# Performance work log

Measured on AMD Instinct MI355X. Metric: run time of the kernel, lower is better.

The kernel has to match this reference:

```python
import jax, jax.numpy as jnp
import numpy as np

EXPERT_NUM = 64
EXPERT_USE = 8
AUX_LOSS_LAMBDA = 0.01


def setup_inputs() -> dict:
    key = jax.random.key(0)
    k1, k2 = jax.random.split(key)
    h = jax.random.normal(k1, (4, 4096, 2048), dtype=jnp.float32)
    # nn.Linear(embed_dim, expert_num) weight: [expert_num, embed_dim], ~U(-1/sqrt(d), 1/sqrt(d))
    bound = 1.0 / np.sqrt(2048.0)
    W = jax.random.uniform(k2, (EXPERT_NUM, 2048), dtype=jnp.float32,
                           minval=-bound, maxval=bound)
    return {"h": h, "W": W}


def reference(h, W):
    b, s, d = h.shape
    hf = h.reshape(-1, d)                              # [b*s, d]
    logits = jnp.einsum('nd,ed->ne', hf, W)            # [b*s, E]
    scores = jax.nn.softmax(logits, axis=-1)           # [b*s, E]
    expert_scores, expert_ids = jax.lax.top_k(scores, EXPERT_USE)  # [b*s, k]
    expert_weight = expert_scores / jnp.sum(expert_scores, axis=-1, keepdims=True)
    # L2 load-balance aux loss (training mode, lambda > 0)
    seq_probs = scores.reshape(b, s, EXPERT_NUM).mean(axis=1)      # [b, E]
    aux_loss = jnp.mean(jnp.sum(seq_probs ** 2, axis=-1)) * EXPERT_NUM * AUX_LOSS_LAMBDA
    return expert_ids, expert_weight, aux_loss
```

## Files before the change

### kernel.cpp

```cpp
#include <hip/hip_runtime.h>
#include <math.h>

#define NTOK 16384
#define DIM 2048
#define NEXP 64
#define TOPK 8
#define BT 32
#define KC 64
#define NCHUNK (DIM / KC)
#define PADK 68
#define NBLK (NTOK / BT)

typedef float f2 __attribute__((ext_vector_type(2)));
typedef float f4 __attribute__((ext_vector_type(4)));

__device__ __forceinline__ f2 pk_mul(f2 a, f2 b) {
    f2 d; asm("v_pk_mul_f32 %0, %1, %2" : "=v"(d) : "v"(a), "v"(b)); return d;
}
__device__ __forceinline__ f2 pk_add(f2 a, f2 b) {
    f2 d; asm("v_pk_add_f32 %0, %1, %2" : "=v"(d) : "v"(a), "v"(b)); return d;
}

__global__ __launch_bounds__(256, 2) void moe_gate_np(
    const float* __restrict__ h, const float* __restrict__ W,
    float* __restrict__ out, float* __restrict__ wsum)
{
#pragma clang fp contract(off)
    __shared__ float sA[BT * PADK];
    __shared__ float sB[NEXP * PADK];
    __shared__ float lg[BT][NEXP + 2];

    const int tid = threadIdx.x;
    const int blk = blockIdx.x;
    const long tok0 = (long)blk * BT;
    const float* hA = h + tok0 * DIM;

    const int rA = tid >> 3;
    const int cA = (tid & 7) * 8;
    const int rB = tid >> 2;
    const int cB = (tid & 3) * 16;

    f4 pa[2], pb[4];
    #pragma unroll
    for (int q = 0; q < 2; ++q) pa[q] = *(const f4*)(hA + (long)rA * DIM + cA + 4 * q);
    #pragma unroll
    for (int q = 0; q < 4; ++q) pb[q] = *(const f4*)(W + (long)rB * DIM + cB + 4 * q);

    const int tx = tid & 15;
    const int ty = tid >> 4;

    f2 axy[2][4], azw[2][4];
    #pragma unroll
    for (int i = 0; i < 2; ++i)
        #pragma unroll
        for (int j = 0; j < 4; ++j) { axy[i][j] = (f2)(0.f); azw[i][j] = (f2)(0.f); }

    for (int kc = 0; kc < NCHUNK; ++kc) {
        __syncthreads();
        #pragma unroll
        for (int q = 0; q < 2; ++q) *(f4*)&sA[rA * PADK + cA + 4 * q] = pa[q];
        #pragma unroll
        for (int q = 0; q < 4; ++q) *(f4*)&sB[rB * PADK + cB + 4 * q] = pb[q];
        __syncthreads();

        if (kc + 1 < NCHUNK) {
            const long ko = (long)(kc + 1) * KC;
            #pragma unroll
            for (int q = 0; q < 2; ++q) pa[q] = *(const f4*)(hA + (long)rA * DIM + ko + cA + 4 * q);
            #pragma unroll
            for (int q = 0; q < 4; ++q) pb[q] = *(const f4*)(W + (long)rB * DIM + ko + cB + 4 * q);
        }

        #pragma unroll
        for (int s = 0; s < 4; ++s) {
            f2 alo[2][4], ahi[2][4], blo[4][4], bhi[4][4];
            #pragma unroll
            for (int i = 0; i < 2; ++i) {
                const float* base = &sA[(ty + 16 * i) * PADK + s * 16];
                #pragma unroll
                for (int v = 0; v < 4; ++v) {
                    f4 a = *(const f4*)(base + 4 * v);
                    alo[i][v] = __builtin_shufflevector(a, a, 0, 1);
                    ahi[i][v] = __builtin_shufflevector(a, a, 2, 3);
                }
            }
            #pragma unroll
            for (int j = 0; j < 4; ++j) {
                const float* base = &sB[(tx + 16 * j) * PADK + s * 16];
                #pragma unroll
                for (int v = 0; v < 4; ++v) {
                    f4 b = *(const f4*)(base + 4 * v);
                    blo[j][v] = __builtin_shufflevector(b, b, 0, 1);
                    bhi[j][v] = __builtin_shufflevector(b, b, 2, 3);
                }
            }
            #pragma unroll
            for (int i = 0; i < 2; ++i)
                #pragma unroll
                for (int j = 0; j < 4; ++j) {
                    f2 t;
                    t = pk_add(pk_mul(alo[i][3], blo[j][3]), axy[i][j]);
                    t = pk_add(pk_mul(alo[i][2], blo[j][2]), t);
                    t = pk_add(pk_mul(alo[i][1], blo[j][1]), t);
                    axy[i][j] = pk_add(pk_mul(alo[i][0], blo[j][0]), t);
                    t = pk_add(pk_mul(ahi[i][3], bhi[j][3]), azw[i][j]);
                    t = pk_add(pk_mul(ahi[i][2], bhi[j][2]), t);
                    t = pk_add(pk_mul(ahi[i][1], bhi[j][1]), t);
                    azw[i][j] = pk_add(pk_mul(ahi[i][0], bhi[j][0]), t);
                }
        }
    }

    #pragma unroll
    for (int i = 0; i < 2; ++i)
        #pragma unroll
        for (int j = 0; j < 4; ++j) {
            f2 s2 = pk_add(axy[i][j], azw[i][j]);
            lg[ty + 16 * i][tx + 16 * j] = s2.x + s2.y;
        }
    __syncthreads();

    const int lane = tid & 63;
    const int wv   = tid >> 6;
    float auxacc = 0.f;

    for (int tt = 0; tt < 8; ++tt) {
        const int t = wv * 8 + tt;
        const float s = lg[t][lane];

        float m = s;
        #pragma unroll
        for (int off = 32; off >= 1; off >>= 1)
            m = fmaxf(m, __shfl_xor(m, off));

        const float p = expf(s - m);
        lg[t][lane] = p;
        __asm__ volatile("" ::: "memory");

        float r0 = lg[t][0], r1 = lg[t][1], r2 = lg[t][2], r3 = lg[t][3];
        float r4 = lg[t][4], r5 = lg[t][5], r6 = lg[t][6], r7 = lg[t][7];
        #pragma unroll
        for (int i = 1; i < 8; ++i) {
            r0 += lg[t][8 * i + 0]; r1 += lg[t][8 * i + 1];
            r2 += lg[t][8 * i + 2]; r3 += lg[t][8 * i + 3];
            r4 += lg[t][8 * i + 4]; r5 += lg[t][8 * i + 5];
            r6 += lg[t][8 * i + 6]; r7 += lg[t][8 * i + 7];
        }
        const float S = ((r0 + r1) + (r2 + r3)) + ((r4 + r5) + (r6 + r7));

        const float score = p / S;
        auxacc += score;

        float cv = score;
        float myv = 0.f;
        int   myi = 0;
        #pragma unroll
        for (int i = 0; i < TOPK; ++i) {
            float v = cv;
            int idx = lane;
            #pragma unroll
            for (int off = 32; off >= 1; off >>= 1) {
                float v2 = __shfl_xor(v, off);
                int   i2 = __shfl_xor(idx, off);
                if (v2 > v || (v2 == v && i2 < idx)) { v = v2; idx = i2; }
            }
            if (lane == i)   { myv = v; myi = idx; }
            if (lane == idx) cv = -1.f;
        }

        float S8 = 0.f;
        #pragma unroll
        for (int r = 0; r < TOPK; ++r) S8 += __shfl(myv, r);

        if (lane < TOPK) {
            const long o = (tok0 + t) * TOPK + lane;
            out[o]                     = (float)myi;
            out[(long)NTOK * TOPK + o] = myv / S8;
        }
    }

    const int b = blk >> 7;
    atomicAdd(&wsum[b * NEXP + lane], auxacc);
}

__global__ void aux_finish(const float* __restrict__ wsum, float* __restrict__ out)
{
    const int lane = threadIdx.x;
    float a = 0.f;
    #pragma unroll
    for (int b = 0; b < 4; ++b) {
        const float v = wsum[b * NEXP + lane] * (1.0f / 4096.0f);
        a = fmaf(v, v, a);
    }
    #pragma unroll
    for (int off = 32; off >= 1; off >>= 1)
        a += __shfl_xor(a, off);
    if (lane == 0)
        out[2L * NTOK * TOPK] = a * 0.25f * (float)NEXP * 0.01f;
}

extern "C" void kernel_launch(void* const* d_in, const int* in_sizes, int n_in,
                              void* d_out, int out_size, void* d_ws, size_t ws_size,
                              hipStream_t stream) {
    const float* h = (const float*)d_in[0];
    const float* W = (const float*)d_in[1];
    float* out  = (float*)d_out;
    float* wsum = (float*)d_ws;

    hipMemsetAsync(d_ws, 0, 1024, stream);
    moe_gate_np<<<NBLK, 256, 0, stream>>>(h, W, out, wsum);
    aux_finish<<<1, 64, 0, stream>>>(wsum, out);
}
```

Before: 165.5 us.

## Shrink gate kernel to single-wave blocks of 16 tokens with 32-wide K chunks

Each block becomes one 64-thread wave that handles 16 tokens instead of 32. Each thread now computes a 4x4 output tile, and the K chunk shrinks to 32 with matching padding, so the block-wide barriers involve only a single wave. The same wave then runs the softmax and top-k for all 16 tokens in sequence. In exchange, each block re-reads the whole expert weight matrix for half as many tokens, the grid holds fewer total waves to hide memory latency, and the serial per-token epilogue gets longer.

```diff
diff --git a/kernel.cpp b/kernel.cpp
--- a/kernel.cpp
+++ b/kernel.cpp
@@ -5,10 +5,10 @@
 #define DIM 2048
 #define NEXP 64
 #define TOPK 8
-#define BT 32
-#define KC 64
+#define BT 16
+#define KC 32
 #define NCHUNK (DIM / KC)
-#define PADK 68
+#define PADK 36
 #define NBLK (NTOK / BT)
 
 typedef float f2 __attribute__((ext_vector_type(2)));
@@ -21,7 +21,7 @@
     f2 d; asm("v_pk_add_f32 %0, %1, %2" : "=v"(d) : "v"(a), "v"(b)); return d;
 }
 
-__global__ __launch_bounds__(256, 2) void moe_gate_np(
+__global__ __launch_bounds__(64, 1) void moe_gate_np(
     const float* __restrict__ h, const float* __restrict__ W,
     float* __restrict__ out, float* __restrict__ wsum)
 {
@@ -35,55 +35,47 @@
     const long tok0 = (long)blk * BT;
     const float* hA = h + tok0 * DIM;
 
-    const int rA = tid >> 3;
-    const int cA = (tid & 7) * 8;
-    const int rB = tid >> 2;
-    const int cB = (tid & 3) * 16;
-
-    f4 pa[2], pb[4];
-    #pragma unroll
-    for (int q = 0; q < 2; ++q) pa[q] = *(const f4*)(hA + (long)rA * DIM + cA + 4 * q);
-    #pragma unroll
-    for (int q = 0; q < 4; ++q) pb[q] = *(const f4*)(W + (long)rB * DIM + cB + 4 * q);
+    const int srow = tid >> 3;
+    const int scol = (tid & 7) * 4;
+
+    f4 pa[2], pb[8];
+    #pragma unroll
+    for (int q = 0; q < 2; ++q)
+        pa[q] = *(const f4*)(hA + (long)(8 * q + srow) * DIM + scol);
+    #pragma unroll
+    for (int q = 0; q < 8; ++q)
+        pb[q] = *(const f4*)(W + (long)(8 * q + srow) * DIM + scol);
 
     const int tx = tid & 15;
     const int ty = tid >> 4;
 
-    f2 axy[2][4], azw[2][4];
-    #pragma unroll
-    for (int i = 0; i < 2; ++i)
+    f2 axy[4][4], azw[4][4];
+    #pragma unroll
+    for (int i = 0; i < 4; ++i)
         #pragma unroll
         for (int j = 0; j < 4; ++j) { axy[i][j] = (f2)(0.f); azw[i][j] = (f2)(0.f); }
 
     for (int kc = 0; kc < NCHUNK; ++kc) {
         __syncthreads();
         #pragma unroll
-        for (int q = 0; q < 2; ++q) *(f4*)&sA[rA * PADK + cA + 4 * q] = pa[q];
-        #pragma unroll
-        for (int q = 0; q < 4; ++q) *(f4*)&sB[rB * PADK + cB + 4 * q] = pb[q];
+        for (int q = 0; q < 2; ++q) *(f4*)&sA[(8 * q + srow) * PADK + scol] = pa[q];
+        #pragma unroll
+        for (int q = 0; q < 8; ++q) *(f4*)&sB[(8 * q + srow) * PADK + scol] = pb[q];
         __syncthreads();
 
         if (kc + 1 < NCHUNK) {
             const long ko = (long)(kc + 1) * KC;
             #pragma unroll
-            for (int q = 0; q < 2; ++q) pa[q] = *(const f4*)(hA + (long)rA * DIM + ko + cA + 4 * q);
-            #pragma unroll
-            for (int q = 0; q < 4; ++q) pb[q] = *(const f4*)(W + (long)rB * DIM + ko + cB + 4 * q);
-        }
-
-        #pragma unroll
-        for (int s = 0; s < 4; ++s) {
-            f2 alo[2][4], ahi[2][4], blo[4][4], bhi[4][4];
-            #pragma unroll
-            for (int i = 0; i < 2; ++i) {
-                const float* base = &sA[(ty + 16 * i) * PADK + s * 16];
-                #pragma unroll
-                for (int v = 0; v < 4; ++v) {
-                    f4 a = *(const f4*)(base + 4 * v);
-                    alo[i][v] = __builtin_shufflevector(a, a, 0, 1);
-                    ahi[i][v] = __builtin_shufflevector(a, a, 2, 3);
-                }
-            }
+            for (int q = 0; q < 2; ++q)
+                pa[q] = *(const f4*)(hA + (long)(8 * q + srow) * DIM + ko + scol);
+            #pragma unroll
+            for (int q = 0; q < 8; ++q)
+                pb[q] = *(const f4*)(W + (long)(8 * q + srow) * DIM + ko + scol);
+        }
+
+        #pragma unroll
+        for (int s = 0; s < 2; ++s) {
+            f2 blo[4][4], bhi[4][4];
             #pragma unroll
             for (int j = 0; j < 4; ++j) {
                 const float* base = &sB[(tx + 16 * j) * PADK + s * 16];
@@ -95,37 +87,46 @@
                 }
             }
             #pragma unroll
-            for (int i = 0; i < 2; ++i)
+            for (int i = 0; i < 4; ++i) {
+                f2 alo[4], ahi[4];
+                const float* base = &sA[(ty + 4 * i) * PADK + s * 16];
+                #pragma unroll
+                for (int v = 0; v < 4; ++v) {
+                    f4 a = *(const f4*)(base + 4 * v);
+                    alo[v] = __builtin_shufflevector(a, a, 0, 1);
+                    ahi[v] = __builtin_shufflevector(a, a, 2, 3);
+                }
                 #pragma unroll
                 for (int j = 0; j < 4; ++j) {
                     f2 t;
-                    t = pk_add(pk_mul(alo[i][3], blo[j][3]), axy[i][j]);
-                    t = pk_add(pk_mul(alo[i][2], blo[j][2]), t);
-                    t = pk_add(pk_mul(alo[i][1], blo[j][1]), t);
-                    axy[i][j] = pk_add(pk_mul(alo[i][0], blo[j][0]), t);
-                    t = pk_add(pk_mul(ahi[i][3], bhi[j][3]), azw[i][j]);
-                    t = pk_add(pk_mul(ahi[i][2], bhi[j][2]), t);
-                    t = pk_add(pk_mul(ahi[i][1], bhi[j][1]), t);
-                    azw[i][j] = pk_add(pk_mul(ahi[i][0], bhi[j][0]), t);
+                    t = pk_add(pk_mul(alo[3], blo[j][3]), axy[i][j]);
+                    t = pk_add(pk_mul(alo[2], blo[j][2]), t);
+                    t = pk_add(pk_mul(alo[1], blo[j][1]), t);
+                    axy[i][j] = pk_add(pk_mul(alo[0], blo[j][0]), t);
+                    t = pk_add(pk_mul(ahi[3], bhi[j][3]), azw[i][j]);
+                    t = pk_add(pk_mul(ahi[2], bhi[j][2]), t);
+                    t = pk_add(pk_mul(ahi[1], bhi[j][1]), t);
+                    azw[i][j] = pk_add(pk_mul(ahi[0], bhi[j][0]), t);
                 }
+            }
         }
     }
 
-    #pragma unroll
-    for (int i = 0; i < 2; ++i)
+    __syncthreads();
+    #pragma unroll
+    for (int i = 0; i < 4; ++i)
         #pragma unroll
         for (int j = 0; j < 4; ++j) {
             f2 s2 = pk_add(axy[i][j], azw[i][j]);
-            lg[ty + 16 * i][tx + 16 * j] = s2.x + s2.y;
+            lg[ty + 4 * i][tx + 16 * j] = s2.x + s2.y;
         }
     __syncthreads();
 
-    const int lane = tid & 63;
-    const int wv   = tid >> 6;
+    const int lane = tid;
     float auxacc = 0.f;
 
-    for (int tt = 0; tt < 8; ++tt) {
-        const int t = wv * 8 + tt;
+    for (int tt = 0; tt < BT; ++tt) {
+        const int t = tt;
         const float s = lg[t][lane];
 
         float m = s;
@@ -179,7 +180,7 @@
         }
     }
 
-    const int b = blk >> 7;
+    const int b = blk >> 8;
     atomicAdd(&wsum[b * NEXP + lane], auxacc);
 }
 
@@ -208,6 +209,6 @@
     float* wsum = (float*)d_ws;
 
     hipMemsetAsync(d_ws, 0, 1024, stream);
-    moe_gate_np<<<NBLK, 256, 0, stream>>>(h, W, out, wsum);
+    moe_gate_np<<<NBLK, 64, 0, stream>>>(h, W, out, wsum);
     aux_finish<<<1, 64, 0, stream>>>(wsum, out);
 }
```

Result: slower. 206.8 us (+25.0%).

## Load h operands directly from global into registers, bypassing shared memory

Applied to the files above, without the earlier changes.

Removes the shared-memory staging tile for the token activations. Each thread now loads its own two token rows straight from global memory into registers, with a one-step register prefetch, while W stays staged through LDS. This cuts LDS traffic and footprint for A. In exchange, 16 lanes now read the same row addresses, which gives uncoalesced or broadcast-dependent global loads and higher register pressure.

```diff
diff --git a/kernel.cpp b/kernel.cpp
--- a/kernel.cpp
+++ b/kernel.cpp
@@ -8,6 +8,7 @@
 #define BT 32
 #define KC 64
 #define NCHUNK (DIM / KC)
+#define NST (DIM / 16)
 #define PADK 68
 #define NBLK (NTOK / BT)
 
@@ -19,6 +20,15 @@
 }
 __device__ __forceinline__ f2 pk_add(f2 a, f2 b) {
     f2 d; asm("v_pk_add_f32 %0, %1, %2" : "=v"(d) : "v"(a), "v"(b)); return d;
+}
+
+__device__ __forceinline__ void loadA(const float* __restrict__ r0,
+                                      const float* __restrict__ r1,
+                                      int kb, f4* dst) {
+    #pragma unroll
+    for (int v = 0; v < 4; ++v) dst[v]     = *(const f4*)(r0 + kb + 4 * v);
+    #pragma unroll
+    for (int v = 0; v < 4; ++v) dst[4 + v] = *(const f4*)(r1 + kb + 4 * v);
 }
 
 __global__ __launch_bounds__(256, 2) void moe_gate_np(
@@ -26,64 +36,55 @@
     float* __restrict__ out, float* __restrict__ wsum)
 {
 #pragma clang fp contract(off)
-    __shared__ float sA[BT * PADK];
     __shared__ float sB[NEXP * PADK];
     __shared__ float lg[BT][NEXP + 2];
 
     const int tid = threadIdx.x;
     const int blk = blockIdx.x;
     const long tok0 = (long)blk * BT;
-    const float* hA = h + tok0 * DIM;
-
-    const int rA = tid >> 3;
-    const int cA = (tid & 7) * 8;
+
     const int rB = tid >> 2;
     const int cB = (tid & 3) * 16;
 
-    f4 pa[2], pb[4];
-    #pragma unroll
-    for (int q = 0; q < 2; ++q) pa[q] = *(const f4*)(hA + (long)rA * DIM + cA + 4 * q);
+    f4 pb[4];
     #pragma unroll
     for (int q = 0; q < 4; ++q) pb[q] = *(const f4*)(W + (long)rB * DIM + cB + 4 * q);
 
     const int tx = tid & 15;
     const int ty = tid >> 4;
 
+    const float* rp0 = h + (tok0 + ty) * DIM;
+    const float* rp1 = h + (tok0 + ty + 16) * DIM;
+
     f2 axy[2][4], azw[2][4];
     #pragma unroll
     for (int i = 0; i < 2; ++i)
         #pragma unroll
         for (int j = 0; j < 4; ++j) { axy[i][j] = (f2)(0.f); azw[i][j] = (f2)(0.f); }
+
+    f4 ca[8], na[8];
+    loadA(rp0, rp1, 0, ca);
 
     for (int kc = 0; kc < NCHUNK; ++kc) {
         __syncthreads();
         #pragma unroll
-        for (int q = 0; q < 2; ++q) *(f4*)&sA[rA * PADK + cA + 4 * q] = pa[q];
-        #pragma unroll
         for (int q = 0; q < 4; ++q) *(f4*)&sB[rB * PADK + cB + 4 * q] = pb[q];
         __syncthreads();
 
         if (kc + 1 < NCHUNK) {
             const long ko = (long)(kc + 1) * KC;
             #pragma unroll
-            for (int q = 0; q < 2; ++q) pa[q] = *(const f4*)(hA + (long)rA * DIM + ko + cA + 4 * q);
-            #pragma unroll
-            for (int q = 0; q < 4; ++q) pb[q] = *(const f4*)(W + (long)rB * DIM + ko + cB + 4 * q);
+            for (int q = 0; q < 4; ++q)
+                pb[q] = *(const f4*)(W + (long)rB * DIM + ko + cB + 4 * q);
         }
 
         #pragma unroll
         for (int s = 0; s < 4; ++s) {
-            f2 alo[2][4], ahi[2][4], blo[4][4], bhi[4][4];
-            #pragma unroll
-            for (int i = 0; i < 2; ++i) {
-                const float* base = &sA[(ty + 16 * i) * PADK + s * 16];
-                #pragma unroll
-                for (int v = 0; v < 4; ++v) {
-                    f4 a = *(const f4*)(base + 4 * v);
-                    alo[i][v] = __builtin_shufflevector(a, a, 0, 1);
-                    ahi[i][v] = __builtin_shufflevector(a, a, 2, 3);
-                }
-            }
+            const int st = kc * 4 + s;
+            if (st + 1 < NST)
+                loadA(rp0, rp1, (st + 1) * 16, na);
+
+            f2 blo[4][4], bhi[4][4];
             #pragma unroll
             for (int j = 0; j < 4; ++j) {
                 const float* base = &sB[(tx + 16 * j) * PADK + s * 16];
@@ -94,23 +95,36 @@
                     bhi[j][v] = __builtin_shufflevector(b, b, 2, 3);
                 }
             }
-            #pragma unroll
-            for (int i = 0; i < 2; ++i)
+
+            #pragma unroll
+            for (int i = 0; i < 2; ++i) {
+                f2 alo[4], ahi[4];
+                #pragma unroll
+                for (int v = 0; v < 4; ++v) {
+                    f4 a = ca[4 * i + v];
+                    alo[v] = __builtin_shufflevector(a, a, 0, 1);
+                    ahi[v] = __builtin_shufflevector(a, a, 2, 3);
+                }
                 #pragma unroll
                 for (int j = 0; j < 4; ++j) {
                     f2 t;
-                    t = pk_add(pk_mul(alo[i][3], blo[j][3]), axy[i][j]);
-                    t = pk_add(pk_mul(alo[i][2], blo[j][2]), t);
-                    t = pk_add(pk_mul(alo[i][1], blo[j][1]), t);
-                    axy[i][j] = pk_add(pk_mul(alo[i][0], blo[j][0]), t);
-                    t = pk_add(pk_mul(ahi[i][3], bhi[j][3]), azw[i][j]);
-                    t = pk_add(pk_mul(ahi[i][2], bhi[j][2]), t);
-                    t = pk_add(pk_mul(ahi[i][1], bhi[j][1]), t);
-                    azw[i][j] = pk_add(pk_mul(ahi[i][0], bhi[j][0]), t);
+                    t = pk_add(pk_mul(alo[3], blo[j][3]), axy[i][j]);
+                    t = pk_add(pk_mul(alo[2], blo[j][2]), t);
+                    t = pk_add(pk_mul(alo[1], blo[j][1]), t);
+                    axy[i][j] = pk_add(pk_mul(alo[0], blo[j][0]), t);
+                    t = pk_add(pk_mul(ahi[3], bhi[j][3]), azw[i][j]);
+                    t = pk_add(pk_mul(ahi[2], bhi[j][2]), t);
+                    t = pk_add(pk_mul(ahi[1], bhi[j][1]), t);
+                    azw[i][j] = pk_add(pk_mul(ahi[0], bhi[j][0]), t);
                 }
+            }
+
+            #pragma unroll
+            for (int q = 0; q < 8; ++q) ca[q] = na[q];
         }
     }
 
+    __syncthreads();
     #pragma unroll
     for (int i = 0; i < 2; ++i)
         #pragma unroll
```

Measured after the change: 170.4 us. 1.03x slower.
